# Kernel optimization log

Measured on AMD Instinct MI355X. Metric: run time of the kernel, lower is better.

The kernel has to match this reference:

```python
import jax, jax.numpy as jnp
import numpy as np

N = 100000      # nodes
E = 1200000     # edges
F_IN = 256      # features_num
HID = 64        # hidden_dim = max(64, 2*32)
NC = 32         # num_class
H = 2           # GAT heads (edge_num < 1.4M)
GAT_SLOPE = 0.2 # GATConv internal LeakyReLU
ACT_SLOPE = 0.01  # F.leaky_relu default


def _glorot(k, shape):
    lim = float(np.sqrt(6.0 / (shape[0] + shape[-1])))
    return jax.random.uniform(k, shape, minval=-lim, maxval=lim, dtype=jnp.float32)


def setup_inputs() -> dict:
    key = jax.random.key(0)
    ks = jax.random.split(key, 32)
    inp = {
        "x": jax.random.normal(ks[0], (N, F_IN), dtype=jnp.float32),
        "edge_index": jax.random.randint(ks[1], (2, E), 0, N, dtype=jnp.int32),
        "edge_weight": jax.random.uniform(ks[2], (E,), dtype=jnp.float32),
    }
    in_dims = [F_IN, 3 * HID]  # layer2 input is cell.output_dim = HID*(1+H)
    ki = 3
    for l, d in enumerate(in_dims):
        inp[f"pre_W{l}"] = _glorot(ks[ki], (d, HID)); ki += 1
        inp[f"pre_b{l}"] = jnp.zeros((HID,), jnp.float32)
        inp[f"gat_W{l}"] = _glorot(ks[ki], (HID, H * HID)); ki += 1
        inp[f"att_src{l}"] = _glorot(ks[ki], (H, HID)); ki += 1
        inp[f"att_dst{l}"] = _glorot(ks[ki], (H, HID)); ki += 1
        inp[f"gat_b{l}"] = jnp.zeros((H * HID,), jnp.float32)
        inp[f"sg_W{l}"] = _glorot(ks[ki], (HID, HID)); ki += 1
        inp[f"sg_b{l}"] = jnp.zeros((HID,), jnp.float32)
    inp["cls_W"] = _glorot(ks[ki], (3 * HID, NC))
    inp["cls_b"] = jnp.zeros((NC,), jnp.float32)
    return inp


def _gat_conv(x, src, dst, W, att_src, att_dst, b):
    # src/dst already include self-loops. x: [N, HID]
    xp = (x @ W).reshape(N, H, HID)                       # [N, H, C]
    a_src = jnp.sum(xp * att_src, axis=-1)                # [N, H]
    a_dst = jnp.sum(xp * att_dst, axis=-1)                # [N, H]
    e = jax.nn.leaky_relu(a_src[src] + a_dst[dst], GAT_SLOPE)  # [E', H]
    m = jax.ops.segment_max(e, dst, num_segments=N)       # segment softmax over dst
    e = jnp.exp(e - m[dst])
    s = jax.ops.segment_sum(e, dst, num_segments=N)
    alpha = e / (s[dst] + 1e-16)
    out = jax.ops.segment_sum(xp[src] * alpha[:, :, None], dst, num_segments=N)
    return out.reshape(N, H * HID) + b


def _sg_conv(x, src_sl, dst_sl, w_sl, W, b):
    # gcn_norm with self-loops (weight 1) already appended; K=1 propagation then linear
    deg = jax.ops.segment_sum(w_sl, dst_sl, num_segments=N)
    dinv = jnp.where(deg > 0, jax.lax.rsqrt(deg), 0.0)
    norm = dinv[src_sl] * w_sl * dinv[dst_sl]             # [E']
    h = jax.ops.segment_sum(x[src_sl] * norm[:, None], dst_sl, num_segments=N)
    return h @ W + b


def _forward(x, edge_index, edge_weight, params):
    src, dst = edge_index[0], edge_index[1]
    loop = jnp.arange(N, dtype=src.dtype)
    src_sl = jnp.concatenate([src, loop])
    dst_sl = jnp.concatenate([dst, loop])
    w_sl = jnp.concatenate([edge_weight, jnp.ones((N,), edge_weight.dtype)])
    for l in range(2):
        pre_W, pre_b, gat_W, a_s, a_d, gat_b, sg_W, sg_b = params[l]
        xh = x @ pre_W + pre_b                            # preprocessor_x
        o1 = jax.nn.leaky_relu(_gat_conv(xh, src_sl, dst_sl, gat_W, a_s, a_d, gat_b), ACT_SLOPE)
        o2 = jax.nn.leaky_relu(_sg_conv(xh, src_sl, dst_sl, w_sl, sg_W, sg_b), ACT_SLOPE)
        x = jax.nn.relu(jnp.concatenate([o1, o2], axis=1))  # [N, 3*HID]
    cls_W, cls_b = params[2]
    logits = x @ cls_W + cls_b
    return jax.nn.log_softmax(logits, axis=-1)


def reference(x, edge_index, edge_weight,
              pre_W0, pre_b0, gat_W0, att_src0, att_dst0, gat_b0, sg_W0, sg_b0,
              pre_W1, pre_b1, gat_W1, att_src1, att_dst1, gat_b1, sg_W1, sg_b1,
              cls_W, cls_b):
    params = [
        (pre_W0, pre_b0, gat_W0, att_src0, att_dst0, gat_b0, sg_W0, sg_b0),
        (pre_W1, pre_b1, gat_W1, att_src1, att_dst1, gat_b1, sg_W1, sg_b1),
        (cls_W, cls_b),
    ]
    return _forward(x, edge_index, edge_weight, params)
```

## Files before the change

### kernel.cpp

```cpp
#include <hip/hip_runtime.h>
#include <hip/hip_fp16.h>
#include <math.h>

#define NN 100000
#define NE 1200000
#define NES (NE + NN)
#define FIN 256
#define NBLK 391

using half8   = __attribute__((ext_vector_type(8))) _Float16;
using floatx4 = __attribute__((ext_vector_type(4))) float;

__device__ __forceinline__ floatx4 mfma16(half8 a, half8 b, floatx4 c) {
    return __builtin_amdgcn_mfma_f32_16x16x32_f16(a, b, c, 0, 0, 0);
}

__global__ __launch_bounds__(256) void k_histdeg(const int* __restrict__ dst,
                                                 const float* __restrict__ ew,
                                                 unsigned long long* __restrict__ packed) {
    int e = blockIdx.x * 256 + threadIdx.x;
    if (e >= NES) return;
    int d; float w;
    if (e < NE) { d = dst[e]; w = ew[e]; } else { d = e - NE; w = 1.f; }
    unsigned long long add = (1ULL << 48)
        + (unsigned long long)((double)w * 4294967296.0);
    atomicAdd(&packed[d], add);
}

__global__ __launch_bounds__(256) void k_scanA(const unsigned long long* __restrict__ packed,
                                               int* __restrict__ row_ptr,
                                               int* __restrict__ bsum,
                                               float* __restrict__ dinv,
                                               int* __restrict__ cur) {
    __shared__ int tmp[256];
    int tid = threadIdx.x;
    int i = blockIdx.x * 256 + tid;
    int v = 0;
    if (i < NN) {
        unsigned long long p = packed[i];
        v = (int)(p >> 48);
        double deg = (double)(p & 0xFFFFFFFFFFFFULL) * (1.0 / 4294967296.0);
        dinv[i] = (deg > 0.0) ? rsqrtf((float)deg) : 0.f;
        cur[i] = 0;
    }
    tmp[tid] = v;
    __syncthreads();
    for (int off = 1; off < 256; off <<= 1) {
        int t = (tid >= off) ? tmp[tid - off] : 0;
        __syncthreads();
        tmp[tid] += t;
        __syncthreads();
    }
    if (i < NN) row_ptr[i] = tmp[tid] - v;
    if (tid == 255) bsum[blockIdx.x] = tmp[255];
}

__global__ __launch_bounds__(512) void k_scanB(int* __restrict__ bsum) {
    __shared__ int tmp[512];
    int tid = threadIdx.x;
    int v = (tid < NBLK) ? bsum[tid] : 0;
    tmp[tid] = v;
    __syncthreads();
    for (int off = 1; off < 512; off <<= 1) {
        int t = (tid >= off) ? tmp[tid - off] : 0;
        __syncthreads();
        tmp[tid] += t;
        __syncthreads();
    }
    if (tid < NBLK) bsum[tid] = tmp[tid] - v;
}

__global__ __launch_bounds__(256) void k_scanC(int* __restrict__ row_ptr,
                                               const int* __restrict__ bsum) {
    int i = blockIdx.x * 256 + threadIdx.x;
    if (i < NN) row_ptr[i] += bsum[i >> 8];
    if (i == 0) row_ptr[NN] = NES;
}

__global__ __launch_bounds__(256) void k_fill(const int* __restrict__ src,
                                              const int* __restrict__ dst,
                                              const float* __restrict__ ew,
                                              const int* __restrict__ row_ptr,
                                              int* __restrict__ cur,
                                              const float* __restrict__ dinv,
                                              int2* __restrict__ recs) {
    int e = blockIdx.x * 256 + threadIdx.x;
    if (e >= NES) return;
    int s, d; float w;
    if (e < NE) { s = src[e]; d = dst[e]; w = ew[e]; } else { s = d = e - NE; w = 1.f; }
    int pos = row_ptr[d] + atomicAdd(&cur[d], 1);
    int2 r; r.x = s; r.y = __float_as_int(w * dinv[s]);
    recs[pos] = r;
}

__global__ __launch_bounds__(256) void k_wconvall(const float* __restrict__ W0,
                                                  const float* __restrict__ W1,
                                                  const float* __restrict__ Wg0,
                                                  const float* __restrict__ Ws0,
                                                  const float* __restrict__ Wg1,
                                                  const float* __restrict__ Ws1,
                                                  const float* __restrict__ Wc,
                                                  const float* __restrict__ As0,
                                                  const float* __restrict__ Ad0,
                                                  const float* __restrict__ As1,
                                                  const float* __restrict__ Ad1,
                                                  __half* __restrict__ Wf,
                                                  float* __restrict__ attf) {
    int o = blockIdx.x * 256 + threadIdx.x;
    if (o >= 59904) return;
    if (o >= 59392) {
        int idx = o - 59392;
        int layer = idx >> 8, rem = idx & 255;
        int v = rem >> 6, c = rem & 63, h = v & 1;
        const float* Wg = layer ? Wg1 : Wg0;
        const float* av = (v < 2) ? (layer ? As1 : As0) : (layer ? Ad1 : Ad0);
        float s = 0.f;
        for (int jj = 0; jj < 64; ++jj)
            s = fmaf(Wg[c * 128 + h * 64 + jj], av[h * 64 + jj], s);
        attf[idx] = s;
        return;
    }
    int lo, NT, N; const float* Wg; const float* Wsg = nullptr;
    if (o < 16384)      { lo = o;         NT = 4;  N = 64; Wg = W0; }
    else if (o < 28672) { lo = o - 16384; NT = 4;  N = 64; Wg = W1; }
    else if (o < 40960) { lo = o - 28672; NT = 12; N = 0;  Wg = Wg0; Wsg = Ws0; }
    else if (o < 53248) { lo = o - 40960; NT = 12; N = 0;  Wg = Wg1; Wsg = Ws1; }
    else                { lo = o - 53248; NT = 2;  N = 32; Wg = Wc; }
    int j = lo & 7, n = (lo >> 3) & 15, q = (lo >> 7) & 3, rest = lo >> 9;
    int t = rest % NT, kc = rest / NT;
    int k = kc * 32 + q * 8 + j, col = t * 16 + n;
    float v;
    if (Wsg) v = (col < 128) ? Wg[(size_t)k * 128 + col] : Wsg[(size_t)k * 64 + (col - 128)];
    else     v = Wg[(size_t)k * N + col];
    Wf[o] = __float2half(v);
}

__device__ __forceinline__ void pre_epi(floatx4* acc, const float* b, const float* attf,
                                        float* a_src, float* a_dst, __half* out,
                                        int rowb, int q, int n) {
    float vs0[4] = {0,0,0,0}, vs1[4] = {0,0,0,0};
    float vd0[4] = {0,0,0,0}, vd1[4] = {0,0,0,0};
    #pragma unroll
    for (int t = 0; t < 4; ++t) {
        float bb  = b[t * 16 + n];
        float ws0 = attf[t * 16 + n],       ws1 = attf[64 + t * 16 + n];
        float wd0 = attf[128 + t * 16 + n], wd1 = attf[192 + t * 16 + n];
        #pragma unroll
        for (int r = 0; r < 4; ++r) {
            float xv = acc[t][r] + bb;
            int row = rowb + q * 4 + r;
            if (row < NN) out[(size_t)row * 64 + t * 16 + n] = __float2half(xv);
            vs0[r] = fmaf(xv, ws0, vs0[r]);
            vs1[r] = fmaf(xv, ws1, vs1[r]);
            vd0[r] = fmaf(xv, wd0, vd0[r]);
            vd1[r] = fmaf(xv, wd1, vd1[r]);
        }
    }
    #pragma unroll
    for (int off = 1; off < 16; off <<= 1) {
        #pragma unroll
        for (int r = 0; r < 4; ++r) {
            vs0[r] += __shfl_xor(vs0[r], off);
            vs1[r] += __shfl_xor(vs1[r], off);
            vd0[r] += __shfl_xor(vd0[r], off);
            vd1[r] += __shfl_xor(vd1[r], off);
        }
    }
    if (n == 0) {
        #pragma unroll
        for (int r = 0; r < 4; ++r) {
            int row = rowb + q * 4 + r;
            if (row < NN) {
                a_src[row * 2]     = vs0[r];
                a_src[row * 2 + 1] = vs1[r];
                a_dst[row * 2]     = vd0[r];
                a_dst[row * 2 + 1] = vd1[r];
            }
        }
    }
}

template<int KK>
__global__ __launch_bounds__(256) void k_pre32(const float* __restrict__ A,
                                               const __half* __restrict__ Wf,
                                               const float* __restrict__ b,
                                               const float* __restrict__ attf,
                                               float* __restrict__ a_src,
                                               float* __restrict__ a_dst,
                                               __half* __restrict__ out) {
    int lane = threadIdx.x & 63, wv = threadIdx.x >> 6;
    int q = lane >> 4, n = lane & 15;
    int rowb = blockIdx.x * 64 + wv * 16;
    int rowA = rowb + n; if (rowA > NN - 1) rowA = NN - 1;
    floatx4 acc[4] = {};
    const float* ap = A + (size_t)rowA * KK + q * 8;
    const __half* wp = Wf + q * 128 + n * 8;
    #pragma unroll
    for (int kc = 0; kc < KK / 32; ++kc) {
        float4 f0 = *(const float4*)(ap + kc * 32);
        float4 f1 = *(const float4*)(ap + kc * 32 + 4);
        half8 a;
        a[0] = (_Float16)f0.x; a[1] = (_Float16)f0.y;
        a[2] = (_Float16)f0.z; a[3] = (_Float16)f0.w;
        a[4] = (_Float16)f1.x; a[5] = (_Float16)f1.y;
        a[6] = (_Float16)f1.z; a[7] = (_Float16)f1.w;
        #pragma unroll
        for (int t = 0; t < 4; ++t) {
            half8 bf = *(const half8*)(wp + (size_t)(kc * 4 + t) * 512);
            acc[t] = mfma16(a, bf, acc[t]);
        }
    }
    pre_epi(acc, b, attf, a_src, a_dst, out, rowb, q, n);
}

__global__ __launch_bounds__(256) void k_pre16(const __half* __restrict__ A,
                                               const __half* __restrict__ Wf,
                                               const float* __restrict__ b,
                                               const float* __restrict__ attf,
                                               float* __restrict__ a_src,
                                               float* __restrict__ a_dst,
                                               __half* __restrict__ out) {
    int lane = threadIdx.x & 63, wv = threadIdx.x >> 6;
    int q = lane >> 4, n = lane & 15;
    int rowb = blockIdx.x * 64 + wv * 16;
    int rowA = rowb + n; if (rowA > NN - 1) rowA = NN - 1;
    floatx4 acc[4] = {};
    const __half* ap = A + (size_t)rowA * 192 + q * 8;
    const __half* wp = Wf + q * 128 + n * 8;
    #pragma unroll
    for (int kc = 0; kc < 6; ++kc) {
        half8 a = *(const half8*)(ap + kc * 32);
        #pragma unroll
        for (int t = 0; t < 4; ++t) {
            half8 bf = *(const half8*)(wp + (size_t)(kc * 4 + t) * 512);
            acc[t] = mfma16(a, bf, acc[t]);
        }
    }
    pre_epi(acc, b, attf, a_src, a_dst, out, rowb, q, n);
}

__global__ __launch_bounds__(256) void k_post(const __half* __restrict__ A,
                                              const __half* __restrict__ Wf,
                                              const float* __restrict__ gat_b,
                                              const float* __restrict__ sg_b,
                                              __half* __restrict__ out) {
    int lane = threadIdx.x & 63, wv = threadIdx.x >> 6;
    int q = lane >> 4, n = lane & 15;
    int rowb = blockIdx.x * 64 + wv * 16;
    int rowA = rowb + n; if (rowA > NN - 1) rowA = NN - 1;
    floatx4 acc[12] = {};
    const __half* ap = A + (size_t)rowA * 192 + q * 8;
    const __half* wp = Wf + q * 128 + n * 8;
    #pragma unroll
    for (int g = 0; g < 3; ++g) {
        #pragma unroll
        for (int kc = 0; kc < 2; ++kc) {
            half8 a = *(const half8*)(ap + g * 64 + kc * 32);
            #pragma unroll
            for (int tt = 0; tt < 4; ++tt) {
                int t = g * 4 + tt;
                half8 bf = *(const half8*)(wp + (size_t)(kc * 12 + t) * 512);
                acc[t] = mfma16(a, bf, acc[t]);
            }
        }
    }
    #pragma unroll
    for (int t = 0; t < 12; ++t) {
        float bb = (t < 8) ? gat_b[t * 16 + n] : sg_b[(t - 8) * 16 + n];
        #pragma unroll
        for (int r = 0; r < 4; ++r) {
            int row = rowb + q * 4 + r;
            if (row < NN)
                out[(size_t)row * 192 + t * 16 + n] =
                    __float2half(fmaxf(acc[t][r] + bb, 0.f));
        }
    }
}

__global__ __launch_bounds__(256) void k_clsm(const __half* __restrict__ A,
                                              const __half* __restrict__ Wf,
                                              const float* __restrict__ b,
                                              float* __restrict__ out) {
    int lane = threadIdx.x & 63, wv = threadIdx.x >> 6;
    int q = lane >> 4, n = lane & 15;
    int rowb = blockIdx.x * 64 + wv * 16;
    int rowA = rowb + n; if (rowA > NN - 1) rowA = NN - 1;
    floatx4 acc[2] = {};
    const __half* ap = A + (size_t)rowA * 192 + q * 8;
    const __half* wp = Wf + q * 128 + n * 8;
    #pragma unroll
    for (int kc = 0; kc < 6; ++kc) {
        half8 a = *(const half8*)(ap + kc * 32);
        #pragma unroll
        for (int t = 0; t < 2; ++t) {
            half8 bf = *(const half8*)(wp + (size_t)(kc * 2 + t) * 512);
            acc[t] = mfma16(a, bf, acc[t]);
        }
    }
    float b0 = b[n], b1 = b[16 + n];
    #pragma unroll
    for (int r = 0; r < 4; ++r) {
        float v0 = acc[0][r] + b0, v1 = acc[1][r] + b1;
        float mx = fmaxf(v0, v1);
        #pragma unroll
        for (int off = 1; off < 16; off <<= 1) mx = fmaxf(mx, __shfl_xor(mx, off));
        float sm = __expf(v0 - mx) + __expf(v1 - mx);
        #pragma unroll
        for (int off = 1; off < 16; off <<= 1) sm += __shfl_xor(sm, off);
        float lg = mx + __logf(sm);
        int row = rowb + q * 4 + r;
        if (row < NN) {
            out[(size_t)row * 32 + n]      = v0 - lg;
            out[(size_t)row * 32 + 16 + n] = v1 - lg;
        }
    }
}

__global__ __launch_bounds__(256) void k_agg(const int* __restrict__ row_ptr,
                                             const int2* __restrict__ recs,
                                             const float* __restrict__ dinv,
                                             const float* __restrict__ a_src,
                                             const float* __restrict__ a_dst,
                                             const __half* __restrict__ xh,
                                             __half* __restrict__ agg) {
    __shared__ float4 einfo[4][64];
    int lane = threadIdx.x & 63;
    int wv = threadIdx.x >> 6;
    int d = blockIdx.x * 4 + wv;
    if (d >= NN) return;
    int p0 = row_ptr[d], p1 = row_ptr[d + 1];
    int nn = p1 - p0;
    float2 ad2 = ((const float2*)a_dst)[d];
    int sub = lane >> 5;
    unsigned flb = (unsigned)(lane & 31) * 4u;

    float g00 = 0.f, g01 = 0.f;
    float g10 = 0.f, g11 = 0.f;
    float s0a = 0.f, s1a = 0.f;

#define EDGE_ACC(E) do {                                                        \
        unsigned off_ = (unsigned)__float_as_int((E).w) + flb;                  \
        float2 v_ = __half22float2(*(const __half2*)((const char*)xh + off_));  \
        g00 = fmaf((E).x, v_.x, g00); g01 = fmaf((E).x, v_.y, g01);             \
        g10 = fmaf((E).y, v_.x, g10); g11 = fmaf((E).y, v_.y, g11);             \
        s0a = fmaf((E).z, v_.x, s0a); s1a = fmaf((E).z, v_.y, s1a);             \
    } while (0)

    if (nn <= 64) {
        float v0 = -INFINITY, v1 = -INFINITY, ewq = 0.f; int es = 0;
        if (lane < nn) {
            int2 rec = recs[p0 + lane];
            es = rec.x;
            ewq = __int_as_float(rec.y);
            float2 a2 = ((const float2*)a_src)[es];
            v0 = a2.x + ad2.x; v0 = (v0 > 0.f) ? v0 : 0.2f * v0;
            v1 = a2.y + ad2.y; v1 = (v1 > 0.f) ? v1 : 0.2f * v1;
        }
        float m0 = v0, m1 = v1;
        #pragma unroll
        for (int off = 32; off; off >>= 1) {
            m0 = fmaxf(m0, __shfl_xor(m0, off));
            m1 = fmaxf(m1, __shfl_xor(m1, off));
        }
        float e0 = (lane < nn) ? __expf(v0 - m0) : 0.f;
        float e1 = (lane < nn) ? __expf(v1 - m1) : 0.f;
        float s0 = e0, s1 = e1;
        #pragma unroll
        for (int off = 32; off; off >>= 1) {
            s0 += __shfl_xor(s0, off);
            s1 += __shfl_xor(s1, off);
        }
        if (lane < nn)
            einfo[wv][lane] = make_float4(e0 / (s0 + 1e-16f), e1 / (s1 + 1e-16f),
                                          ewq, __int_as_float(es << 7));
        const float4* ep = &einfo[wv][sub];
        int j = 0;
        for (; j + 4 <= nn; j += 4) {
            float4 eA = ep[j];
            float4 eB = ep[j + 2];
            EDGE_ACC(eA);
            EDGE_ACC(eB);
        }
        for (; j + 2 <= nn; j += 2) {
            float4 eA = ep[j];
            EDGE_ACC(eA);
        }
        if (nn & 1) {
            if (sub == 0) {
                float4 eT = einfo[wv][nn - 1];
                EDGE_ACC(eT);
            }
        }
    } else {
        float m0 = -INFINITY, m1 = -INFINITY;
        for (int e = p0 + lane; e < p1; e += 64) {
            int s = recs[e].x;
            float2 a2 = ((const float2*)a_src)[s];
            float v0 = a2.x + ad2.x; v0 = (v0 > 0.f) ? v0 : 0.2f * v0;
            float v1 = a2.y + ad2.y; v1 = (v1 > 0.f) ? v1 : 0.2f * v1;
            m0 = fmaxf(m0, v0); m1 = fmaxf(m1, v1);
        }
        #pragma unroll
        for (int off = 32; off; off >>= 1) {
            m0 = fmaxf(m0, __shfl_xor(m0, off));
            m1 = fmaxf(m1, __shfl_xor(m1, off));
        }
        float s0 = 0.f, s1 = 0.f;
        for (int e = p0 + lane; e < p1; e += 64) {
            int s = recs[e].x;
            float2 a2 = ((const float2*)a_src)[s];
            float v0 = a2.x + ad2.x; v0 = (v0 > 0.f) ? v0 : 0.2f * v0;
            float v1 = a2.y + ad2.y; v1 = (v1 > 0.f) ? v1 : 0.2f * v1;
            s0 += __expf(v0 - m0); s1 += __expf(v1 - m1);
        }
        #pragma unroll
        for (int off = 32; off; off >>= 1) {
            s0 += __shfl_xor(s0, off);
            s1 += __shfl_xor(s1, off);
        }
        float inv0 = 1.f / (s0 + 1e-16f), inv1 = 1.f / (s1 + 1e-16f);
        for (int base = p0; base < p1; base += 64) {
            int e = base + lane;
            int nc = min(64, p1 - base);
            if (e < p1) {
                int2 rec = recs[e];
                int es = rec.x;
                float ewq = __int_as_float(rec.y);
                float2 a2 = ((const float2*)a_src)[es];
                float v0 = a2.x + ad2.x; v0 = (v0 > 0.f) ? v0 : 0.2f * v0;
                float v1 = a2.y + ad2.y; v1 = (v1 > 0.f) ? v1 : 0.2f * v1;
                einfo[wv][lane] = make_float4(__expf(v0 - m0) * inv0,
                                              __expf(v1 - m1) * inv1,
                                              ewq, __int_as_float(es << 7));
            }
            const float4* ep = &einfo[wv][sub];
            int j = 0;
            for (; j + 2 <= nc; j += 2) {
                float4 eA = ep[j];
                EDGE_ACC(eA);
            }
            if (nc & 1) {
                if (sub == 0) {
                    float4 eT = einfo[wv][nc - 1];
                    EDGE_ACC(eT);
                }
            }
        }
    }
#undef EDGE_ACC

    g00 += __shfl_xor(g00, 32); g01 += __shfl_xor(g01, 32);
    g10 += __shfl_xor(g10, 32); g11 += __shfl_xor(g11, 32);
    s0a += __shfl_xor(s0a, 32); s1a += __shfl_xor(s1a, 32);

    float did = dinv[d];
    __half* op = agg + (size_t)d * 192;
    int fp = (lane & 31) * 2;
    if (lane < 32) {
        *(__half2*)(op + fp)       = __floats2half2_rn(g00, g01);
        *(__half2*)(op + 128 + fp) = __floats2half2_rn(s0a * did, s1a * did);
    } else {
        *(__half2*)(op + 64 + fp)  = __floats2half2_rn(g10, g11);
    }
}

extern "C" void kernel_launch(void* const* d_in, const int* in_sizes, int n_in,
                              void* d_out, int out_size, void* d_ws, size_t ws_size,
                              hipStream_t stream) {
    const float* x   = (const float*)d_in[0];
    const int*   ei  = (const int*)d_in[1];
    const float* ew  = (const float*)d_in[2];
    const int* src = ei;
    const int* dst = ei + NE;

    const float* P[2][8];
    for (int l = 0; l < 2; ++l)
        for (int j = 0; j < 8; ++j)
            P[l][j] = (const float*)d_in[3 + l * 8 + j];
    const float* cls_W = (const float*)d_in[19];
    const float* cls_b = (const float*)d_in[20];

    float* ws = (float*)d_ws;
    const size_t n = NN;
    __half* xh_h = (__half*)(ws);
    __half* agg  = (__half*)(ws + 32 * n);
    float* a_src = ws + 128 * n;
    float* a_dst = ws + 130 * n;
    __half* xA_h = (__half*)(ws + 132 * n);
    __half* xB_h = (__half*)(ws + 228 * n);
    __half* Wf   = (__half*)(ws + 324 * n);
    float* attf  = ws + 324 * n + 29696;
    float* base2 = ws + 324 * n + 29696 + 512;
    unsigned long long* packed = (unsigned long long*)base2;
    int*   cur        = (int*)(packed + NN);
    float* dinv       = (float*)(cur + NN);
    int*   row_ptr    = (int*)(dinv + NN);
    int*   bsum       = row_ptr + (NN + 1);
    int2*  recs       = (int2*)(bsum + 513);

    __half* Wf_pre0 = Wf;
    __half* Wf_pre1 = Wf + 16384;
    __half* Wf_pq0  = Wf + 28672;
    __half* Wf_pq1  = Wf + 40960;
    __half* Wf_cls  = Wf + 53248;

    const int TB = 256;
    int gb_edge  = (NES + TB - 1) / TB;
    int gb_node  = (NN + TB - 1) / TB;
    int gb_wave4 = (NN + 3) / 4;
    int gb64     = (NN + 63) / 64;

    k_wconvall<<<(59904 + TB - 1) / TB, TB, 0, stream>>>(
        P[0][0], P[1][0], P[0][2], P[0][6], P[1][2], P[1][6], cls_W,
        P[0][3], P[0][4], P[1][3], P[1][4], Wf, attf);

    hipMemsetAsync(packed, 0, NN * sizeof(unsigned long long), stream);
    k_histdeg<<<gb_edge, TB, 0, stream>>>(dst, ew, packed);
    k_scanA<<<NBLK, TB, 0, stream>>>(packed, row_ptr, bsum, dinv, cur);
    k_scanB<<<1, 512, 0, stream>>>(bsum);
    k_scanC<<<gb_node, TB, 0, stream>>>(row_ptr, bsum);
    k_fill <<<gb_edge, TB, 0, stream>>>(src, dst, ew, row_ptr, cur, dinv, recs);

    for (int l = 0; l < 2; ++l) {
        const float* pre_b = P[l][1];
        const float* gat_b = P[l][5];
        const float* sg_b  = P[l][7];
        __half* xout = (l == 0) ? xA_h : xB_h;

        if (l == 0)
            k_pre32<256><<<gb64, TB, 0, stream>>>(x, Wf_pre0, pre_b,
                                                  attf, a_src, a_dst, xh_h);
        else
            k_pre16<<<gb64, TB, 0, stream>>>(xA_h, Wf_pre1, pre_b,
                                             attf + 256, a_src, a_dst, xh_h);
        k_agg <<<gb_wave4, TB, 0, stream>>>(row_ptr, recs, dinv,
                                            a_src, a_dst, xh_h, agg);
        k_post<<<gb64, TB, 0, stream>>>(agg, (l == 0) ? Wf_pq0 : Wf_pq1,
                                        gat_b, sg_b, xout);
    }

    k_clsm<<<gb64, TB, 0, stream>>>(xB_h, Wf_cls, cls_b, (float*)d_out);
}
```

Baseline: 538.0 us.

## Fuse histogram with weight conversion, reuse atomic slot order, handle self-loops implicitly

The degree histogram now records each edge's slot from the atomicAdd's old value and runs in the same launch as the weight conversion. This removes the second atomic pass in the CSR fill, the cur array and one kernel launch. Self-loops are no longer stored in the CSR; the aggregation kernel adds them analytically. a_src and dinv are packed into one float4 per node so each neighbour costs a single gather, with the symmetric normalisation applied at aggregation time. The price is extra branching in the aggregation kernel, a 4M-byte ord array, and a dense path limit lowered to 63 neighbours.

Result: faster. 501.9 us (-6.7%).

```diff
diff --git a/kernel.cpp b/kernel.cpp
--- a/kernel.cpp
+++ b/kernel.cpp
@@ -4,9 +4,9 @@
 
 #define NN 100000
 #define NE 1200000
-#define NES (NE + NN)
 #define FIN 256
 #define NBLK 391
+#define HB 4688
 
 using half8   = __attribute__((ext_vector_type(8))) _Float16;
 using floatx4 = __attribute__((ext_vector_type(4))) float;
@@ -15,98 +15,35 @@
     return __builtin_amdgcn_mfma_f32_16x16x32_f16(a, b, c, 0, 0, 0);
 }
 
-__global__ __launch_bounds__(256) void k_histdeg(const int* __restrict__ dst,
-                                                 const float* __restrict__ ew,
-                                                 unsigned long long* __restrict__ packed) {
-    int e = blockIdx.x * 256 + threadIdx.x;
-    if (e >= NES) return;
-    int d; float w;
-    if (e < NE) { d = dst[e]; w = ew[e]; } else { d = e - NE; w = 1.f; }
-    unsigned long long add = (1ULL << 48)
-        + (unsigned long long)((double)w * 4294967296.0);
-    atomicAdd(&packed[d], add);
-}
-
-__global__ __launch_bounds__(256) void k_scanA(const unsigned long long* __restrict__ packed,
-                                               int* __restrict__ row_ptr,
-                                               int* __restrict__ bsum,
-                                               float* __restrict__ dinv,
-                                               int* __restrict__ cur) {
-    __shared__ int tmp[256];
-    int tid = threadIdx.x;
-    int i = blockIdx.x * 256 + tid;
-    int v = 0;
-    if (i < NN) {
-        unsigned long long p = packed[i];
-        v = (int)(p >> 48);
-        double deg = (double)(p & 0xFFFFFFFFFFFFULL) * (1.0 / 4294967296.0);
-        dinv[i] = (deg > 0.0) ? rsqrtf((float)deg) : 0.f;
-        cur[i] = 0;
-    }
-    tmp[tid] = v;
-    __syncthreads();
-    for (int off = 1; off < 256; off <<= 1) {
-        int t = (tid >= off) ? tmp[tid - off] : 0;
-        __syncthreads();
-        tmp[tid] += t;
-        __syncthreads();
-    }
-    if (i < NN) row_ptr[i] = tmp[tid] - v;
-    if (tid == 255) bsum[blockIdx.x] = tmp[255];
-}
-
-__global__ __launch_bounds__(512) void k_scanB(int* __restrict__ bsum) {
-    __shared__ int tmp[512];
-    int tid = threadIdx.x;
-    int v = (tid < NBLK) ? bsum[tid] : 0;
-    tmp[tid] = v;
-    __syncthreads();
-    for (int off = 1; off < 512; off <<= 1) {
-        int t = (tid >= off) ? tmp[tid - off] : 0;
-        __syncthreads();
-        tmp[tid] += t;
-        __syncthreads();
-    }
-    if (tid < NBLK) bsum[tid] = tmp[tid] - v;
-}
-
-__global__ __launch_bounds__(256) void k_scanC(int* __restrict__ row_ptr,
-                                               const int* __restrict__ bsum) {
-    int i = blockIdx.x * 256 + threadIdx.x;
-    if (i < NN) row_ptr[i] += bsum[i >> 8];
-    if (i == 0) row_ptr[NN] = NES;
-}
-
-__global__ __launch_bounds__(256) void k_fill(const int* __restrict__ src,
-                                              const int* __restrict__ dst,
+__global__ __launch_bounds__(256) void k_prep(const int* __restrict__ dst,
                                               const float* __restrict__ ew,
-                                              const int* __restrict__ row_ptr,
-                                              int* __restrict__ cur,
-                                              const float* __restrict__ dinv,
-                                              int2* __restrict__ recs) {
-    int e = blockIdx.x * 256 + threadIdx.x;
-    if (e >= NES) return;
-    int s, d; float w;
-    if (e < NE) { s = src[e]; d = dst[e]; w = ew[e]; } else { s = d = e - NE; w = 1.f; }
-    int pos = row_ptr[d] + atomicAdd(&cur[d], 1);
-    int2 r; r.x = s; r.y = __float_as_int(w * dinv[s]);
-    recs[pos] = r;
-}
-
-__global__ __launch_bounds__(256) void k_wconvall(const float* __restrict__ W0,
-                                                  const float* __restrict__ W1,
-                                                  const float* __restrict__ Wg0,
-                                                  const float* __restrict__ Ws0,
-                                                  const float* __restrict__ Wg1,
-                                                  const float* __restrict__ Ws1,
-                                                  const float* __restrict__ Wc,
-                                                  const float* __restrict__ As0,
-                                                  const float* __restrict__ Ad0,
-                                                  const float* __restrict__ As1,
-                                                  const float* __restrict__ Ad1,
-                                                  __half* __restrict__ Wf,
-                                                  float* __restrict__ attf) {
-    int o = blockIdx.x * 256 + threadIdx.x;
+                                              unsigned long long* __restrict__ packed,
+                                              int* __restrict__ ord,
+                                              const float* __restrict__ W0,
+                                              const float* __restrict__ W1,
+                                              const float* __restrict__ Wg0,
+                                              const float* __restrict__ Ws0,
+                                              const float* __restrict__ Wg1,
+                                              const float* __restrict__ Ws1,
+                                              const float* __restrict__ Wc,
+                                              const float* __restrict__ As0,
+                                              const float* __restrict__ Ad0,
+                                              const float* __restrict__ As1,
+                                              const float* __restrict__ Ad1,
+                                              __half* __restrict__ Wf,
+                                              float* __restrict__ attf) {
+    int bid = blockIdx.x;
+    if (bid < HB) {
+        int e = bid * 256 + threadIdx.x;
+        if (e >= NE) return;
+        int d = dst[e]; float w = ew[e];
+        unsigned long long add = (1ULL << 48)
+            + (unsigned long long)((double)w * 4294967296.0);
+        unsigned long long old = atomicAdd(&packed[d], add);
+        ord[e] = (int)(old >> 48);
+        return;
+    }
+    int o = (bid - HB) * 256 + threadIdx.x;
     if (o >= 59904) return;
     if (o >= 59392) {
         int idx = o - 59392;
@@ -135,8 +72,70 @@
     Wf[o] = __float2half(v);
 }
 
+__global__ __launch_bounds__(256) void k_scanA(const unsigned long long* __restrict__ packed,
+                                               int* __restrict__ row_ptr,
+                                               int* __restrict__ bsum,
+                                               float* __restrict__ asd) {
+    __shared__ int tmp[256];
+    int tid = threadIdx.x;
+    int i = blockIdx.x * 256 + tid;
+    int v = 0;
+    if (i < NN) {
+        unsigned long long p = packed[i];
+        v = (int)(p >> 48);
+        double deg = (double)(p & 0xFFFFFFFFFFFFULL) * (1.0 / 4294967296.0) + 1.0;
+        asd[i * 4 + 2] = rsqrtf((float)deg);
+    }
+    tmp[tid] = v;
+    __syncthreads();
+    for (int off = 1; off < 256; off <<= 1) {
+        int t = (tid >= off) ? tmp[tid - off] : 0;
+        __syncthreads();
+        tmp[tid] += t;
+        __syncthreads();
+    }
+    if (i < NN) row_ptr[i] = tmp[tid] - v;
+    if (tid == 255) bsum[blockIdx.x] = tmp[255];
+}
+
+__global__ __launch_bounds__(512) void k_scanB(int* __restrict__ bsum) {
+    __shared__ int tmp[512];
+    int tid = threadIdx.x;
+    int v = (tid < NBLK) ? bsum[tid] : 0;
+    tmp[tid] = v;
+    __syncthreads();
+    for (int off = 1; off < 512; off <<= 1) {
+        int t = (tid >= off) ? tmp[tid - off] : 0;
+        __syncthreads();
+        tmp[tid] += t;
+        __syncthreads();
+    }
+    if (tid < NBLK) bsum[tid] = tmp[tid] - v;
+}
+
+__global__ __launch_bounds__(256) void k_scanC(int* __restrict__ row_ptr,
+                                               const int* __restrict__ bsum) {
+    int i = blockIdx.x * 256 + threadIdx.x;
+    if (i < NN) row_ptr[i] += bsum[i >> 8];
+    if (i == 0) row_ptr[NN] = NE;
+}
+
+__global__ __launch_bounds__(256) void k_fill(const int* __restrict__ src,
+                                              const int* __restrict__ dst,
+                                              const float* __restrict__ ew,
+                                              const int* __restrict__ row_ptr,
+                                              const int* __restrict__ ord,
+                                              int2* __restrict__ recs) {
+    int e = blockIdx.x * 256 + threadIdx.x;
+    if (e >= NE) return;
+    int d = dst[e];
+    int pos = row_ptr[d] + ord[e];
+    int2 r; r.x = src[e]; r.y = __float_as_int(ew[e]);
+    recs[pos] = r;
+}
+
 __device__ __forceinline__ void pre_epi(floatx4* acc, const float* b, const float* attf,
-                                        float* a_src, float* a_dst, __half* out,
+                                        float* asd, float* a_dst, __half* out,
                                         int rowb, int q, int n) {
     float vs0[4] = {0,0,0,0}, vs1[4] = {0,0,0,0};
     float vd0[4] = {0,0,0,0}, vd1[4] = {0,0,0,0};
@@ -171,10 +170,8 @@
         for (int r = 0; r < 4; ++r) {
             int row = rowb + q * 4 + r;
             if (row < NN) {
-                a_src[row * 2]     = vs0[r];
-                a_src[row * 2 + 1] = vs1[r];
-                a_dst[row * 2]     = vd0[r];
-                a_dst[row * 2 + 1] = vd1[r];
+                *(float2*)&asd[row * 4] = make_float2(vs0[r], vs1[r]);
+                *(float2*)&a_dst[row * 2] = make_float2(vd0[r], vd1[r]);
             }
         }
     }
@@ -185,7 +182,7 @@
                                                const __half* __restrict__ Wf,
                                                const float* __restrict__ b,
                                                const float* __restrict__ attf,
-                                               float* __restrict__ a_src,
+                                               float* __restrict__ asd,
                                                float* __restrict__ a_dst,
                                                __half* __restrict__ out) {
     int lane = threadIdx.x & 63, wv = threadIdx.x >> 6;
@@ -210,14 +207,14 @@
             acc[t] = mfma16(a, bf, acc[t]);
         }
     }
-    pre_epi(acc, b, attf, a_src, a_dst, out, rowb, q, n);
+    pre_epi(acc, b, attf, asd, a_dst, out, rowb, q, n);
 }
 
 __global__ __launch_bounds__(256) void k_pre16(const __half* __restrict__ A,
                                                const __half* __restrict__ Wf,
                                                const float* __restrict__ b,
                                                const float* __restrict__ attf,
-                                               float* __restrict__ a_src,
+                                               float* __restrict__ asd,
                                                float* __restrict__ a_dst,
                                                __half* __restrict__ out) {
     int lane = threadIdx.x & 63, wv = threadIdx.x >> 6;
@@ -236,7 +233,7 @@
             acc[t] = mfma16(a, bf, acc[t]);
         }
     }
-    pre_epi(acc, b, attf, a_src, a_dst, out, rowb, q, n);
+    pre_epi(acc, b, attf, asd, a_dst, out, rowb, q, n);
 }
 
 __global__ __launch_bounds__(256) void k_post(const __half* __restrict__ A,
@@ -318,8 +315,7 @@
 
 __global__ __launch_bounds__(256) void k_agg(const int* __restrict__ row_ptr,
                                              const int2* __restrict__ recs,
-                                             const float* __restrict__ dinv,
-                                             const float* __restrict__ a_src,
+                                             const float* __restrict__ asd,
                                              const float* __restrict__ a_dst,
                                              const __half* __restrict__ xh,
                                              __half* __restrict__ agg) {
@@ -331,6 +327,7 @@
     int p0 = row_ptr[d], p1 = row_ptr[d + 1];
     int nn = p1 - p0;
     float2 ad2 = ((const float2*)a_dst)[d];
+    const float4* asd4 = (const float4*)asd;
     int sub = lane >> 5;
     unsigned flb = (unsigned)(lane & 31) * 4u;
 
@@ -346,15 +343,20 @@
         s0a = fmaf((E).z, v_.x, s0a); s1a = fmaf((E).z, v_.y, s1a);             \
     } while (0)
 
-    if (nn <= 64) {
+    if (nn <= 63) {
+        int tot = nn + 1;
         float v0 = -INFINITY, v1 = -INFINITY, ewq = 0.f; int es = 0;
-        if (lane < nn) {
-            int2 rec = recs[p0 + lane];
-            es = rec.x;
-            ewq = __int_as_float(rec.y);
-            float2 a2 = ((const float2*)a_src)[es];
-            v0 = a2.x + ad2.x; v0 = (v0 > 0.f) ? v0 : 0.2f * v0;
-            v1 = a2.y + ad2.y; v1 = (v1 > 0.f) ? v1 : 0.2f * v1;
+        if (lane < tot) {
+            float wraw;
+            if (lane < nn) {
+                int2 rec = recs[p0 + lane];
+                es = rec.x;
+                wraw = __int_as_float(rec.y);
+            } else { es = d; wraw = 1.f; }
+            float4 a4 = asd4[es];
+            v0 = a4.x + ad2.x; v0 = (v0 > 0.f) ? v0 : 0.2f * v0;
+            v1 = a4.y + ad2.y; v1 = (v1 > 0.f) ? v1 : 0.2f * v1;
+            ewq = wraw * a4.z;
         }
         float m0 = v0, m1 = v1;
         #pragma unroll
@@ -362,42 +364,45 @@
             m0 = fmaxf(m0, __shfl_xor(m0, off));
             m1 = fmaxf(m1, __shfl_xor(m1, off));
         }
-        float e0 = (lane < nn) ? __expf(v0 - m0) : 0.f;
-        float e1 = (lane < nn) ? __expf(v1 - m1) : 0.f;
+        float e0 = (lane < tot) ? __expf(v0 - m0) : 0.f;
+        float e1 = (lane < tot) ? __expf(v1 - m1) : 0.f;
         float s0 = e0, s1 = e1;
         #pragma unroll
         for (int off = 32; off; off >>= 1) {
             s0 += __shfl_xor(s0, off);
             s1 += __shfl_xor(s1, off);
         }
-        if (lane < nn)
+        if (lane < tot)
             einfo[wv][lane] = make_float4(e0 / (s0 + 1e-16f), e1 / (s1 + 1e-16f),
                                           ewq, __int_as_float(es << 7));
         const float4* ep = &einfo[wv][sub];
         int j = 0;
-        for (; j + 4 <= nn; j += 4) {
+        for (; j + 4 <= tot; j += 4) {
             float4 eA = ep[j];
             float4 eB = ep[j + 2];
             EDGE_ACC(eA);
             EDGE_ACC(eB);
         }
-        for (; j + 2 <= nn; j += 2) {
+        for (; j + 2 <= tot; j += 2) {
             float4 eA = ep[j];
             EDGE_ACC(eA);
         }
-        if (nn & 1) {
+        if (tot & 1) {
             if (sub == 0) {
-                float4 eT = einfo[wv][nn - 1];
+                float4 eT = einfo[wv][tot - 1];
                 EDGE_ACC(eT);
             }
         }
     } else {
-        float m0 = -INFINITY, m1 = -INFINITY;
+        float4 aself = asd4[d];
+        float sv0 = aself.x + ad2.x; sv0 = (sv0 > 0.f) ? sv0 : 0.2f * sv0;
+        float sv1 = aself.y + ad2.y; sv1 = (sv1 > 0.f) ? sv1 : 0.2f * sv1;
+        float m0 = sv0, m1 = sv1;
         for (int e = p0 + lane; e < p1; e += 64) {
             int s = recs[e].x;
-            float2 a2 = ((const float2*)a_src)[s];
-            float v0 = a2.x + ad2.x; v0 = (v0 > 0.f) ? v0 : 0.2f * v0;
-            float v1 = a2.y + ad2.y; v1 = (v1 > 0.f) ? v1 : 0.2f * v1;
+            float4 a4 = asd4[s];
+            float v0 = a4.x + ad2.x; v0 = (v0 > 0.f) ? v0 : 0.2f * v0;
+            float v1 = a4.y + ad2.y; v1 = (v1 > 0.f) ? v1 : 0.2f * v1;
             m0 = fmaxf(m0, v0); m1 = fmaxf(m1, v1);
         }
         #pragma unroll
@@ -408,9 +413,9 @@
         float s0 = 0.f, s1 = 0.f;
         for (int e = p0 + lane; e < p1; e += 64) {
             int s = recs[e].x;
-            float2 a2 = ((const float2*)a_src)[s];
-            float v0 = a2.x + ad2.x; v0 = (v0 > 0.f) ? v0 : 0.2f * v0;
-            float v1 = a2.y + ad2.y; v1 = (v1 > 0.f) ? v1 : 0.2f * v1;
+            float4 a4 = asd4[s];
+            float v0 = a4.x + ad2.x; v0 = (v0 > 0.f) ? v0 : 0.2f * v0;
+            float v1 = a4.y + ad2.y; v1 = (v1 > 0.f) ? v1 : 0.2f * v1;
             s0 += __expf(v0 - m0); s1 += __expf(v1 - m1);
         }
         #pragma unroll
@@ -418,6 +423,7 @@
             s0 += __shfl_xor(s0, off);
             s1 += __shfl_xor(s1, off);
         }
+        s0 += __expf(sv0 - m0); s1 += __expf(sv1 - m1);
         float inv0 = 1.f / (s0 + 1e-16f), inv1 = 1.f / (s1 + 1e-16f);
         for (int base = p0; base < p1; base += 64) {
             int e = base + lane;
@@ -425,13 +431,13 @@
             if (e < p1) {
                 int2 rec = recs[e];
                 int es = rec.x;
-                float ewq = __int_as_float(rec.y);
-                float2 a2 = ((const float2*)a_src)[es];
-                float v0 = a2.x + ad2.x; v0 = (v0 > 0.f) ? v0 : 0.2f * v0;
-                float v1 = a2.y + ad2.y; v1 = (v1 > 0.f) ? v1 : 0.2f * v1;
+                float4 a4 = asd4[es];
+                float v0 = a4.x + ad2.x; v0 = (v0 > 0.f) ? v0 : 0.2f * v0;
+                float v1 = a4.y + ad2.y; v1 = (v1 > 0.f) ? v1 : 0.2f * v1;
                 einfo[wv][lane] = make_float4(__expf(v0 - m0) * inv0,
                                               __expf(v1 - m1) * inv1,
-                                              ewq, __int_as_float(es << 7));
+                                              __int_as_float(rec.y) * a4.z,
+                                              __int_as_float(es << 7));
             }
             const float4* ep = &einfo[wv][sub];
             int j = 0;
@@ -446,6 +452,12 @@
                 }
             }
         }
+        if (sub == 0) {
+            float4 eS = make_float4(__expf(sv0 - m0) * inv0,
+                                    __expf(sv1 - m1) * inv1,
+                                    aself.z, __int_as_float(d << 7));
+            EDGE_ACC(eS);
+        }
     }
 #undef EDGE_ACC
 
@@ -453,7 +465,7 @@
     g10 += __shfl_xor(g10, 32); g11 += __shfl_xor(g11, 32);
     s0a += __shfl_xor(s0a, 32); s1a += __shfl_xor(s1a, 32);
 
-    float did = dinv[d];
+    float did = asd[d * 4 + 2];
     __half* op = agg + (size_t)d * 192;
     int fp = (lane & 31) * 2;
     if (lane < 32) {
@@ -484,19 +496,18 @@
     const size_t n = NN;
     __half* xh_h = (__half*)(ws);
     __half* agg  = (__half*)(ws + 32 * n);
-    float* a_src = ws + 128 * n;
-    float* a_dst = ws + 130 * n;
-    __half* xA_h = (__half*)(ws + 132 * n);
-    __half* xB_h = (__half*)(ws + 228 * n);
-    __half* Wf   = (__half*)(ws + 324 * n);
-    float* attf  = ws + 324 * n + 29696;
-    float* base2 = ws + 324 * n + 29696 + 512;
+    float* asd   = ws + 128 * n;
+    float* a_dst = ws + 132 * n;
+    __half* xA_h = (__half*)(ws + 134 * n);
+    __half* xB_h = (__half*)(ws + 230 * n);
+    __half* Wf   = (__half*)(ws + 326 * n);
+    float* attf  = ws + 326 * n + 29696;
+    float* base2 = ws + 326 * n + 30208;
     unsigned long long* packed = (unsigned long long*)base2;
-    int*   cur        = (int*)(packed + NN);
-    float* dinv       = (float*)(cur + NN);
-    int*   row_ptr    = (int*)(dinv + NN);
+    int*   row_ptr    = (int*)(packed + NN);
     int*   bsum       = row_ptr + (NN + 1);
-    int2*  recs       = (int2*)(bsum + 513);
+    int*   ord        = bsum + 513;
+    int2*  recs       = (int2*)(ord + NE);
 
     __half* Wf_pre0 = Wf;
     __half* Wf_pre1 = Wf + 16384;
@@ -505,21 +516,21 @@
     __half* Wf_cls  = Wf + 53248;
 
     const int TB = 256;
-    int gb_edge  = (NES + TB - 1) / TB;
+    int gb_edge  = (NE + TB - 1) / TB;
     int gb_node  = (NN + TB - 1) / TB;
     int gb_wave4 = (NN + 3) / 4;
     int gb64     = (NN + 63) / 64;
 
-    k_wconvall<<<(59904 + TB - 1) / TB, TB, 0, stream>>>(
+    hipMemsetAsync(packed, 0, NN * sizeof(unsigned long long), stream);
+    k_prep<<<HB + (59904 + TB - 1) / TB, TB, 0, stream>>>(
+        dst, ew, packed, ord,
         P[0][0], P[1][0], P[0][2], P[0][6], P[1][2], P[1][6], cls_W,
         P[0][3], P[0][4], P[1][3], P[1][4], Wf, attf);
 
-    hipMemsetAsync(packed, 0, NN * sizeof(unsigned long long), stream);
-    k_histdeg<<<gb_edge, TB, 0, stream>>>(dst, ew, packed);
-    k_scanA<<<NBLK, TB, 0, stream>>>(packed, row_ptr, bsum, dinv, cur);
+    k_scanA<<<NBLK, TB, 0, stream>>>(packed, row_ptr, bsum, asd);
     k_scanB<<<1, 512, 0, stream>>>(bsum);
     k_scanC<<<gb_node, TB, 0, stream>>>(row_ptr, bsum);
-    k_fill <<<gb_edge, TB, 0, stream>>>(src, dst, ew, row_ptr, cur, dinv, recs);
+    k_fill <<<gb_edge, TB, 0, stream>>>(src, dst, ew, row_ptr, ord, recs);
 
     for (int l = 0; l < 2; ++l) {
         const float* pre_b = P[l][1];
@@ -529,12 +540,11 @@
 
         if (l == 0)
             k_pre32<256><<<gb64, TB, 0, stream>>>(x, Wf_pre0, pre_b,
-                                                  attf, a_src, a_dst, xh_h);
+                                                  attf, asd, a_dst, xh_h);
         else
             k_pre16<<<gb64, TB, 0, stream>>>(xA_h, Wf_pre1, pre_b,
-                                             attf + 256, a_src, a_dst, xh_h);
-        k_agg <<<gb_wave4, TB, 0, stream>>>(row_ptr, recs, dinv,
-                                            a_src, a_dst, xh_h, agg);
+                                             attf + 256, asd, a_dst, xh_h);
+        k_agg <<<gb_wave4, TB, 0, stream>>>(row_ptr, recs, asd, a_dst, xh_h, agg);
         k_post<<<gb64, TB, 0, stream>>>(agg, (l == 0) ? Wf_pq0 : Wf_pq1,
                                         gat_b, sg_b, xout);
     }
```
